# Optimization experiments

Hardware: AMD Instinct MI355X
Metric: run time of the kernel (lower is better)

Reference implementation:

```python
import jax, jax.numpy as jnp
import numpy as np

D_MODEL = 1024
N_HEADS = 16


def setup_inputs() -> dict:
    key = jax.random.key(0)
    ks = jax.random.split(key, 5)
    B, T, C = 4, 2048, D_MODEL
    x = jax.random.normal(ks[0], (B, T, C), dtype=jnp.float32)
    W_attn = jax.random.normal(ks[1], (C, 3 * C), dtype=jnp.float32) * (1.0 / np.sqrt(C))
    b_attn = jnp.zeros((3 * C,), dtype=jnp.float32)
    W_proj = jax.random.normal(ks[2], (C, C), dtype=jnp.float32) * (1.0 / np.sqrt(C))
    b_proj = jnp.zeros((C,), dtype=jnp.float32)
    return {"x": x, "W_attn": W_attn, "b_attn": b_attn, "W_proj": W_proj, "b_proj": b_proj}


def reference(x, W_attn, b_attn, W_proj, b_proj):
    B, T, C = x.shape
    H = N_HEADS
    hd = C // H
    qkv = x @ W_attn + b_attn                      # [B,T,3C]
    q, k, v = jnp.split(qkv, 3, axis=2)
    # [B,T,C] -> [B,H,T,hd]
    q = q.reshape(B, T, H, hd).transpose(0, 2, 1, 3)
    k = k.reshape(B, T, H, hd).transpose(0, 2, 1, 3)
    v = v.reshape(B, T, H, hd).transpose(0, 2, 1, 3)
    scale = 1.0 / jnp.sqrt(jnp.float32(hd))
    attn = jnp.einsum('bhqd,bhkd->bhqk', q, k) * scale
    causal = jnp.tril(jnp.ones((T, T), dtype=bool))
    attn = jnp.where(causal[None, None], attn, -jnp.inf)
    w = jax.nn.softmax(attn, axis=-1)
    ctx = jnp.einsum('bhqk,bhkd->bhqd', w, v)      # [B,H,T,hd]
    ctx = ctx.transpose(0, 2, 1, 3).reshape(B, T, C)
    return ctx @ W_proj + b_proj
```

## Files before the change

kernel.cpp:

```cpp
#include <hip/hip_runtime.h>
#include <hip/hip_bf16.h>

typedef __bf16 bf16x8 __attribute__((ext_vector_type(8)));
typedef __bf16 bf16x4 __attribute__((ext_vector_type(4)));
typedef float f32x4 __attribute__((ext_vector_type(4)));

#define MFMA(A, B, C) __builtin_amdgcn_mfma_f32_16x16x32_bf16((A), (B), (C), 0, 0, 0)

#if __has_builtin(__builtin_amdgcn_exp2f)
#define EXP2(x) __builtin_amdgcn_exp2f(x)
#else
#define EXP2(x) exp2f(x)
#endif

#define T_SEQ 2048
#define BATCH 4
#define CDIM  1024
#define HEADS 16
#define HD    64
#define MROWS (BATCH * T_SEQ)
#define QK_SCALE 0.18033688011112042f
#define KTILES (CDIM / 64)

__device__ __forceinline__ void async_ld16(const __bf16* g, __bf16* l) {
    __builtin_amdgcn_global_load_lds(
        (const __attribute__((address_space(1))) void*)g,
        (__attribute__((address_space(3))) void*)l, 16, 0, 0);
}

__global__ __launch_bounds__(256) void prep(const float* __restrict__ x,
                                            __bf16* __restrict__ xbf,
                                            const float* __restrict__ Wa,
                                            __bf16* __restrict__ Wat)
{
    __shared__ float tile[32][33];
    const int bid = blockIdx.x;
    if (bid < 4096) {
        long i = ((long)bid * 256 + threadIdx.x) * 8;
        f32x4 f0 = ((const f32x4*)(x + i))[0];
        f32x4 f1 = ((const f32x4*)(x + i))[1];
        bf16x8 v;
#pragma unroll
        for (int j = 0; j < 4; j++) { v[j] = (__bf16)f0[j]; v[4 + j] = (__bf16)f1[j]; }
        *(bf16x8*)(xbf + i) = v;
    } else {
        const int bb = bid - 4096;
        const int tx = threadIdx.x & 31, ty = threadIdx.x >> 5;
        const int c0 = (bb % 96) * 32, r0 = (bb / 96) * 32;
#pragma unroll
        for (int i = 0; i < 4; i++)
            tile[ty + i * 8][tx] = Wa[(long)(r0 + ty + i * 8) * (3 * CDIM) + c0 + tx];
        __syncthreads();
#pragma unroll
        for (int i = 0; i < 4; i++)
            Wat[(long)(c0 + ty + i * 8) * CDIM + r0 + tx] = (__bf16)tile[tx][ty + i * 8];
    }
}

__global__ __launch_bounds__(256) void conv_transpose(const float* __restrict__ src,
                                                      __bf16* __restrict__ dst,
                                                      int R, int C)
{
    __shared__ float tile[32][33];
    int c0 = blockIdx.x * 32, r0 = blockIdx.y * 32;
    int tx = threadIdx.x, ty = threadIdx.y;
#pragma unroll
    for (int i = 0; i < 4; i++)
        tile[ty + i * 8][tx] = src[(long)(r0 + ty + i * 8) * C + c0 + tx];
    __syncthreads();
#pragma unroll
    for (int i = 0; i < 4; i++)
        dst[(long)(c0 + ty + i * 8) * R + r0 + tx] = (__bf16)tile[tx][ty + i * 8];
}


#define QS_ALO(p, kt)                                                            \
    do {                                                                         \
        async_ld16(Asrc + (long)(kt) * 64, &Ab[p][sdst]);                        \
        async_ld16(Asrc + (long)128 * CDIM + (kt) * 64, &Ab[p][8192 + sdst]);    \
    } while (0)
#define QS_AHI(p, kt)                                                            \
    do {                                                                         \
        async_ld16(Asrc + (long)64 * CDIM + (kt) * 64, &Ab[p][4096 + sdst]);     \
        async_ld16(Asrc + (long)192 * CDIM + (kt) * 64, &Ab[p][12288 + sdst]);   \
    } while (0)
#define QS_B(p, kt)                                                              \
    do {                                                                         \
        async_ld16(Bsrc + (long)(kt) * 64, &Bb[p][sdst]);                        \
        async_ld16(Bsrc + (long)64 * CDIM + (kt) * 64, &Bb[p][4096 + sdst]);     \
        async_ld16(Bsrc + (long)128 * CDIM + (kt) * 64, &Bb[p][8192 + sdst]);    \
    } while (0)

__global__ __launch_bounds__(512, 2) void gemm_qkv(const __bf16* __restrict__ A,
                                                   const __bf16* __restrict__ Bt,
                                                   const float* __restrict__ bias,
                                                   __bf16* __restrict__ C,
                                                   __bf16* __restrict__ vt)
{
    __shared__ __attribute__((aligned(16))) __bf16 Ab[2][256 * 64];
    __shared__ __attribute__((aligned(16))) __bf16 Bb[2][192 * 64];

    const int bid = (int)blockIdx.x;
    const int swz = (bid & 7) * 64 + (bid >> 3);
    const int n0 = (swz & 15) * 192;
    const int m0 = (swz >> 4) * 256;

    const int t = threadIdx.x;
    const int wave = t >> 6, lane = t & 63;
    const int quad = lane >> 4, l15 = lane & 15;
    const int wm = wave >> 2, wn = wave & 3;

    const int srow = t >> 3;
    const int scol = ((t & 7) * 8) ^ ((srow & 7) << 3);
    const int sdst = srow * 64 + (t & 7) * 8;
    const __bf16* Asrc = A + (long)(m0 + srow) * CDIM + scol;
    const __bf16* Bsrc = Bt + (long)(n0 + srow) * CDIM + scol;

    const int kx0 = (quad * 8) ^ ((l15 & 7) << 3);
    const int kx1 = (32 + quad * 8) ^ ((l15 & 7) << 3);
    const int aro = (wm * 128 + l15) * 64;
    const int bro = (wn * 48 + l15) * 64;

    f32x4 acc[8][3] = {};
    bf16x8 A0[4][2], A1[4][2], B0[2][2], B1[2];

    QS_ALO(0, 0); QS_AHI(0, 0); QS_B(0, 0);
    QS_ALO(1, 1); QS_AHI(1, 1); QS_B(1, 1);
    asm volatile("s_waitcnt vmcnt(7)" ::: "memory");
    __builtin_amdgcn_s_barrier();
#pragma unroll
    for (int mf = 0; mf < 4; mf++) {
        A0[mf][0] = *(const bf16x8*)&Ab[0][aro + mf * 1024 + kx0];
        A0[mf][1] = *(const bf16x8*)&Ab[0][aro + mf * 1024 + kx1];
    }
#pragma unroll
    for (int nf = 0; nf < 2; nf++) {
        B0[nf][0] = *(const bf16x8*)&Bb[0][bro + nf * 1024 + kx0];
        B0[nf][1] = *(const bf16x8*)&Bb[0][bro + nf * 1024 + kx1];
    }

#pragma unroll 2
    for (int kt = 0; kt < KTILES; ++kt) {
        const int cur = kt & 1, nxt = cur ^ 1;

#pragma unroll
        for (int mf = 0; mf < 4; mf++) {
            A1[mf][0] = *(const bf16x8*)&Ab[cur][aro + 4096 + mf * 1024 + kx0];
            A1[mf][1] = *(const bf16x8*)&Ab[cur][aro + 4096 + mf * 1024 + kx1];
        }
        __builtin_amdgcn_s_barrier();
        asm volatile("s_waitcnt lgkmcnt(8)");
        __builtin_amdgcn_sched_barrier(0);
        __builtin_amdgcn_s_setprio(1);
#pragma unroll
        for (int mf = 0; mf < 4; mf++)
#pragma unroll
            for (int nf = 0; nf < 2; nf++) {
                acc[mf][nf] = MFMA(A0[mf][0], B0[nf][0], acc[mf][nf]);
                acc[mf][nf] = MFMA(A0[mf][1], B0[nf][1], acc[mf][nf]);
            }
        __builtin_amdgcn_s_setprio(0);
        __builtin_amdgcn_s_barrier();

        B1[0] = *(const bf16x8*)&Bb[cur][bro + 2048 + kx0];
        B1[1] = *(const bf16x8*)&Bb[cur][bro + 2048 + kx1];
        if (kt + 2 < KTILES) QS_ALO(cur, kt + 2);
        __builtin_amdgcn_s_barrier();
        asm volatile("s_waitcnt lgkmcnt(2)");
        __builtin_amdgcn_sched_barrier(0);
        __builtin_amdgcn_s_setprio(1);
#pragma unroll
        for (int mf = 0; mf < 4; mf++)
#pragma unroll
            for (int nf = 0; nf < 2; nf++) {
                acc[4 + mf][nf] = MFMA(A1[mf][0], B0[nf][0], acc[4 + mf][nf]);
                acc[4 + mf][nf] = MFMA(A1[mf][1], B0[nf][1], acc[4 + mf][nf]);
            }
        __builtin_amdgcn_s_setprio(0);
        if (kt + 2 < KTILES) { asm volatile("s_waitcnt vmcnt(2)" ::: "memory"); }
        else                 { asm volatile("s_waitcnt vmcnt(0)" ::: "memory"); }
        __builtin_amdgcn_s_barrier();

        if (kt + 2 < KTILES) QS_AHI(cur, kt + 2);
        if (kt + 1 < KTILES) {
#pragma unroll
            for (int nf = 0; nf < 2; nf++) {
                B0[nf][0] = *(const bf16x8*)&Bb[nxt][bro + nf * 1024 + kx0];
                B0[nf][1] = *(const bf16x8*)&Bb[nxt][bro + nf * 1024 + kx1];
            }
        }
        __builtin_amdgcn_s_barrier();
        asm volatile("s_waitcnt lgkmcnt(4)");
        __builtin_amdgcn_sched_barrier(0);
        __builtin_amdgcn_s_setprio(1);
#pragma unroll
        for (int mf = 0; mf < 4; mf++) {
            acc[mf][2] = MFMA(A0[mf][0], B1[0], acc[mf][2]);
            acc[mf][2] = MFMA(A0[mf][1], B1[1], acc[mf][2]);
        }
        __builtin_amdgcn_s_setprio(0);
        __builtin_amdgcn_s_barrier();

        if (kt + 2 < KTILES) QS_B(cur, kt + 2);
        if (kt + 1 < KTILES) {
#pragma unroll
            for (int mf = 0; mf < 4; mf++) {
                A0[mf][0] = *(const bf16x8*)&Ab[nxt][aro + mf * 1024 + kx0];
                A0[mf][1] = *(const bf16x8*)&Ab[nxt][aro + mf * 1024 + kx1];
            }
        }
        __builtin_amdgcn_s_barrier();
        asm volatile("s_waitcnt lgkmcnt(8)");
        __builtin_amdgcn_sched_barrier(0);
        __builtin_amdgcn_s_setprio(1);
#pragma unroll
        for (int mf = 0; mf < 4; mf++) {
            acc[4 + mf][2] = MFMA(A1[mf][0], B1[0], acc[4 + mf][2]);
            acc[4 + mf][2] = MFMA(A1[mf][1], B1[1], acc[4 + mf][2]);
        }
        __builtin_amdgcn_s_setprio(0);
        __builtin_amdgcn_s_barrier();
    }

    const int bB = m0 >> 11;
    const int tb = (m0 & (T_SEQ - 1)) + wm * 128;
#pragma unroll
    for (int mf = 0; mf < 8; mf++) {
#pragma unroll
        for (int nf = 0; nf < 3; nf++) {
            const int colb = n0 + wn * 48 + nf * 16;
            const int col = colb + l15;
            const float bv = bias[col];
            if (colb >= 2 * CDIM) {
                __bf16* vdst = vt + (long)(bB * CDIM + col - 2 * CDIM) * T_SEQ
                             + tb + (mf >> 2) * 64 + (mf & 3) * 16 + quad * 4;
                bf16x4 pv;
#pragma unroll
                for (int r = 0; r < 4; r++) pv[r] = (__bf16)(acc[mf][nf][r] + bv);
                *(bf16x4*)vdst = pv;
            } else {
                const float sc = (col < CDIM) ? QK_SCALE : 1.0f;
#pragma unroll
                for (int r = 0; r < 4; r++) {
                    const int row = m0 + wm * 128 + (mf >> 2) * 64 + (mf & 3) * 16 + quad * 4 + r;
                    C[(long)row * (3 * CDIM) + col] = (__bf16)((acc[mf][nf][r] + bv) * sc);
                }
            }
        }
    }
}

#define PS_A(p, kt)                                                              \
    do {                                                                         \
        async_ld16(Asrc + (long)(kt) * 64, &Ab[p][sdst]);                        \
        async_ld16(Asrc + (long)64 * (3 * CDIM) + (kt) * 64, &Ab[p][4096 + sdst]); \
    } while (0)
#define PS_B(p, kt)                                                              \
    do {                                                                         \
        async_ld16(Bsrc + (long)(kt) * 64, &Bb[p][sdst]);                        \
        async_ld16(Bsrc + (long)64 * CDIM + (kt) * 64, &Bb[p][4096 + sdst]);     \
        async_ld16(Bsrc + (long)128 * CDIM + (kt) * 64, &Bb[p][8192 + sdst]);    \
        async_ld16(Bsrc + (long)192 * CDIM + (kt) * 64, &Bb[p][12288 + sdst]);   \
    } while (0)

__global__ __launch_bounds__(512, 2) void gemm_proj(const __bf16* __restrict__ A,
                                                    const __bf16* __restrict__ Bt,
                                                    const float* __restrict__ bias,
                                                    float* __restrict__ C)
{
    __shared__ __attribute__((aligned(16))) __bf16 Ab[2][128 * 64];
    __shared__ __attribute__((aligned(16))) __bf16 Bb[2][256 * 64];

    const int bid = (int)blockIdx.x;
    const int swz = (bid & 7) * 32 + (bid >> 3);
    const int n0 = (swz & 3) * 256;
    const int m0 = (swz >> 2) * 128;

    const int t = threadIdx.x;
    const int wave = t >> 6, lane = t & 63;
    const int quad = lane >> 4, l15 = lane & 15;
    const int wm = wave >> 2, wn = wave & 3;

    const int srow = t >> 3;
    const int scol = ((t & 7) * 8) ^ ((srow & 7) << 3);
    const int sdst = srow * 64 + (t & 7) * 8;
    const __bf16* Asrc = A + (long)(m0 + srow) * (3 * CDIM) + scol;
    const __bf16* Bsrc = Bt + (long)(n0 + srow) * CDIM + scol;

    const int kx0 = (quad * 8) ^ ((l15 & 7) << 3);
    const int kx1 = (32 + quad * 8) ^ ((l15 & 7) << 3);
    const int aro = (wm * 64 + l15) * 64;
    const int bro = (wn * 64 + l15) * 64;

    f32x4 acc[4][4] = {};
    bf16x8 A0[2][2], A1[2][2], B0[2][2], B1[2][2];

    PS_A(0, 0); PS_B(0, 0);
    PS_A(1, 1); PS_B(1, 1);
    asm volatile("s_waitcnt vmcnt(6)" ::: "memory");
    __builtin_amdgcn_s_barrier();
#pragma unroll
    for (int mf = 0; mf < 2; mf++) {
        A0[mf][0] = *(const bf16x8*)&Ab[0][aro + mf * 1024 + kx0];
        A0[mf][1] = *(const bf16x8*)&Ab[0][aro + mf * 1024 + kx1];
    }
#pragma unroll
    for (int nf = 0; nf < 2; nf++) {
        B0[nf][0] = *(const bf16x8*)&Bb[0][bro + nf * 1024 + kx0];
        B0[nf][1] = *(const bf16x8*)&Bb[0][bro + nf * 1024 + kx1];
    }

#pragma unroll 2
    for (int kt = 0; kt < KTILES; ++kt) {
        const int cur = kt & 1, nxt = cur ^ 1;

#pragma unroll
        for (int mf = 0; mf < 2; mf++) {
            A1[mf][0] = *(const bf16x8*)&Ab[cur][aro + 2048 + mf * 1024 + kx0];
            A1[mf][1] = *(const bf16x8*)&Ab[cur][aro + 2048 + mf * 1024 + kx1];
        }
        __builtin_amdgcn_s_barrier();
        asm volatile("s_waitcnt lgkmcnt(4)");
        __builtin_amdgcn_sched_barrier(0);
        __builtin_amdgcn_s_setprio(1);
#pragma unroll
        for (int mf = 0; mf < 2; mf++)
#pragma unroll
            for (int nf = 0; nf < 2; nf++) {
                acc[mf][nf] = MFMA(A0[mf][0], B0[nf][0], acc[mf][nf]);
                acc[mf][nf] = MFMA(A0[mf][1], B0[nf][1], acc[mf][nf]);
            }
        __builtin_amdgcn_s_setprio(0);
        __builtin_amdgcn_s_barrier();

#pragma unroll
        for (int nf = 0; nf < 2; nf++) {
            B1[nf][0] = *(const bf16x8*)&Bb[cur][bro + 2048 + nf * 1024 + kx0];
            B1[nf][1] = *(const bf16x8*)&Bb[cur][bro + 2048 + nf * 1024 + kx1];
        }
        __builtin_amdgcn_s_barrier();
        asm volatile("s_waitcnt lgkmcnt(4)");
        __builtin_amdgcn_sched_barrier(0);
        __builtin_amdgcn_s_setprio(1);
#pragma unroll
        for (int mf = 0; mf < 2; mf++)
#pragma unroll
            for (int nf = 0; nf < 2; nf++) {
                acc[2 + mf][nf] = MFMA(A1[mf][0], B0[nf][0], acc[2 + mf][nf]);
                acc[2 + mf][nf] = MFMA(A1[mf][1], B0[nf][1], acc[2 + mf][nf]);
            }
        __builtin_amdgcn_s_setprio(0);
        asm volatile("s_waitcnt vmcnt(0)" ::: "memory");
        __builtin_amdgcn_s_barrier();

        if (kt + 2 < KTILES) PS_A(cur, kt + 2);
        if (kt + 1 < KTILES) {
#pragma unroll
            for (int nf = 0; nf < 2; nf++) {
                B0[nf][0] = *(const bf16x8*)&Bb[nxt][bro + nf * 1024 + kx0];
                B0[nf][1] = *(const bf16x8*)&Bb[nxt][bro + nf * 1024 + kx1];
            }
        }
        __builtin_amdgcn_s_barrier();
        asm volatile("s_waitcnt lgkmcnt(4)");
        __builtin_amdgcn_sched_barrier(0);
        __builtin_amdgcn_s_setprio(1);
#pragma unroll
        for (int mf = 0; mf < 2; mf++)
#pragma unroll
            for (int nf = 0; nf < 2; nf++) {
                acc[mf][2 + nf] = MFMA(A0[mf][0], B1[nf][0], acc[mf][2 + nf]);
                acc[mf][2 + nf] = MFMA(A0[mf][1], B1[nf][1], acc[mf][2 + nf]);
            }
        __builtin_amdgcn_s_setprio(0);
        __builtin_amdgcn_s_barrier();

        if (kt + 2 < KTILES) PS_B(cur, kt + 2);
        if (kt + 1 < KTILES) {
#pragma unroll
            for (int mf = 0; mf < 2; mf++) {
                A0[mf][0] = *(const bf16x8*)&Ab[nxt][aro + mf * 1024 + kx0];
                A0[mf][1] = *(const bf16x8*)&Ab[nxt][aro + mf * 1024 + kx1];
            }
        }
        __builtin_amdgcn_s_barrier();
        asm volatile("s_waitcnt lgkmcnt(4)");
        __builtin_amdgcn_sched_barrier(0);
        __builtin_amdgcn_s_setprio(1);
#pragma unroll
        for (int mf = 0; mf < 2; mf++)
#pragma unroll
            for (int nf = 0; nf < 2; nf++) {
                acc[2 + mf][2 + nf] = MFMA(A1[mf][0], B1[nf][0], acc[2 + mf][2 + nf]);
                acc[2 + mf][2 + nf] = MFMA(A1[mf][1], B1[nf][1], acc[2 + mf][2 + nf]);
            }
        __builtin_amdgcn_s_setprio(0);
        __builtin_amdgcn_s_barrier();
    }

#pragma unroll
    for (int mf = 0; mf < 4; mf++) {
#pragma unroll
        for (int nf = 0; nf < 4; nf++) {
            const int col = n0 + wn * 64 + (nf >> 1) * 32 + (nf & 1) * 16 + l15;
            const float bv = bias[col];
#pragma unroll
            for (int r = 0; r < 4; r++) {
                const int row = m0 + wm * 64 + (mf >> 1) * 32 + (mf & 1) * 16 + quad * 4 + r;
                C[(long)row * CDIM + col] = acc[mf][nf][r] + bv;
            }
        }
    }
}

__global__ __launch_bounds__(256) void attn_kernel(__bf16* qkv,
                                                   const __bf16* __restrict__ vt)
{
    __shared__ __attribute__((aligned(16))) __bf16 Ks[2][64 * 32];
    __shared__ __attribute__((aligned(16))) __bf16 Vts[2][64 * 32];
    __shared__ __attribute__((aligned(16))) __bf16 Ps[8][16 * 72];

    const int bh = blockIdx.x;
    const int b = bh >> 4, h = bh & 15;
    const int qt = (int)gridDim.y - 1 - (int)blockIdx.y;
    const int q0 = qt * 128;
    const int t = threadIdx.x;
    const int wave = t >> 6, lane = t & 63;
    const int quad = lane >> 4, l15 = lane & 15;

    bf16x8 qfr[2][2];
#pragma unroll
    for (int f = 0; f < 2; f++) {
        const __bf16* qb = qkv + (long)(b * T_SEQ + q0 + f * 64 + wave * 16 + l15) * (3 * CDIM) + h * HD;
        qfr[f][0] = *(const bf16x8*)(qb + quad * 8);
        qfr[f][1] = *(const bf16x8*)(qb + 32 + quad * 8);
    }

    bf16x8 vone;
#pragma unroll
    for (int j = 0; j < 8; j++) vone[j] = (__bf16)1.0f;

    f32x4 Oacc[2][4] = {};
    f32x4 lacc[2] = {};

    const __bf16* kbase = qkv + (long)(b * T_SEQ + (t >> 2)) * (3 * CDIM)
                          + CDIM + h * HD + (t & 3) * 8;
    const __bf16* vbase = vt + ((long)bh * HD + (t >> 2)) * T_SEQ + (t & 3) * 8;

    const int ntiles = (q0 + 128) / 64;
    for (int kt = 0; kt < ntiles; kt++) {
        const __bf16* kp = kbase + (long)kt * 64 * (3 * CDIM);
        async_ld16(kp,      &Ks[0][t * 8]);
        async_ld16(kp + 32, &Ks[1][t * 8]);
        const __bf16* vp = vbase + kt * 64;
        async_ld16(vp,      &Vts[0][t * 8]);
        async_ld16(vp + 32, &Vts[1][t * 8]);
        __syncthreads();

#pragma unroll
        for (int c = 0; c < 4; c++) {
            bf16x8 kf0 = *(const bf16x8*)&Ks[0][(c * 16 + l15) * 32 + quad * 8];
            bf16x8 kf1 = *(const bf16x8*)&Ks[1][(c * 16 + l15) * 32 + quad * 8];
#pragma unroll
            for (int f = 0; f < 2; f++) {
                f32x4 z = {};
                z = MFMA(kf0, qfr[f][0], z);
                z = MFMA(kf1, qfr[f][1], z);
                const int qbf = q0 + f * 64 + wave * 16;
                const int qg = qbf + l15;
                const int kvb = kt * 64 + c * 16 + quad * 4;
                bf16x4 pk;
                if (kt * 64 + 63 > qbf) {
#pragma unroll
                    for (int r = 0; r < 4; r++) {
                        float v = (kvb + r > qg) ? -1e30f : z[r];
                        pk[r] = (__bf16)EXP2(v);
                    }
                } else {
#pragma unroll
                    for (int r = 0; r < 4; r++)
                        pk[r] = (__bf16)EXP2(z[r]);
                }
                *(bf16x4*)&Ps[wave * 2 + f][l15 * 72 + c * 16 + quad * 4] = pk;
            }
        }

        __threadfence_block();

        bf16x8 pf[2][2];
#pragma unroll
        for (int f = 0; f < 2; f++) {
            pf[f][0] = *(const bf16x8*)&Ps[wave * 2 + f][l15 * 72 + quad * 8];
            pf[f][1] = *(const bf16x8*)&Ps[wave * 2 + f][l15 * 72 + 32 + quad * 8];
            lacc[f] = MFMA(pf[f][0], vone, lacc[f]);
            lacc[f] = MFMA(pf[f][1], vone, lacc[f]);
        }
#pragma unroll
        for (int n = 0; n < 4; n++) {
            bf16x8 vf0 = *(const bf16x8*)&Vts[0][(n * 16 + l15) * 32 + quad * 8];
            bf16x8 vf1 = *(const bf16x8*)&Vts[1][(n * 16 + l15) * 32 + quad * 8];
#pragma unroll
            for (int f = 0; f < 2; f++) {
                Oacc[f][n] = MFMA(pf[f][0], vf0, Oacc[f][n]);
                Oacc[f][n] = MFMA(pf[f][1], vf1, Oacc[f][n]);
            }
        }
        __syncthreads();
    }

#pragma unroll
    for (int f = 0; f < 2; f++)
#pragma unroll
        for (int n = 0; n < 4; n++) {
            int col = h * HD + n * 16 + l15;
#pragma unroll
            for (int r = 0; r < 4; r++) {
                int row = q0 + f * 64 + wave * 16 + quad * 4 + r;
                float val = Oacc[f][n][r] / lacc[f][r];
                qkv[(long)(b * T_SEQ + row) * (3 * CDIM) + col] = (__bf16)val;
            }
        }
}

extern "C" void kernel_launch(void* const* d_in, const int* in_sizes, int n_in,
                              void* d_out, int out_size, void* d_ws, size_t ws_size,
                              hipStream_t stream) {
    (void)in_sizes; (void)n_in; (void)out_size; (void)ws_size;
    const float* x  = (const float*)d_in[0];
    const float* Wa = (const float*)d_in[1];
    const float* ba = (const float*)d_in[2];
    const float* Wp = (const float*)d_in[3];
    const float* bp = (const float*)d_in[4];
    float* out = (float*)d_out;

    char* ws = (char*)d_ws;
    __bf16* qkv = (__bf16*)(ws);
    __bf16* vt  = (__bf16*)(ws + 50331648);
    __bf16* Wpt = (__bf16*)(ws + 50331648);
    __bf16* xbf = (__bf16*)d_out;
    __bf16* Wat = (__bf16*)((char*)d_out + 16777216);

    prep<<<dim3(4096 + 3072), 256, 0, stream>>>(x, xbf, Wa, Wat);

    gemm_qkv<<<dim3(512), 512, 0, stream>>>(xbf, Wat, ba, qkv, vt);

    attn_kernel<<<dim3(BATCH * HEADS, T_SEQ / 128), 256, 0, stream>>>(qkv, vt);

    conv_transpose<<<dim3(CDIM / 32, CDIM / 32), dim3(32, 8), 0, stream>>>(Wp, Wpt, CDIM, CDIM);

    gemm_proj<<<dim3(256), 512, 0, stream>>>(qkv, Wpt, bp, out);
}
```

Measured before the change: 249.8 us.

## Fold Wproj transpose into prep and stage V-transpose stores through LDS

New measurement: 251.4 us. Within noise of the previous version (+0.7%).

```diff
diff --git a/kernel.cpp b/kernel.cpp
--- a/kernel.cpp
+++ b/kernel.cpp
@@ -31,7 +31,9 @@
 __global__ __launch_bounds__(256) void prep(const float* __restrict__ x,
                                             __bf16* __restrict__ xbf,
                                             const float* __restrict__ Wa,
-                                            __bf16* __restrict__ Wat)
+                                            __bf16* __restrict__ Wat,
+                                            const float* __restrict__ Wp,
+                                            __bf16* __restrict__ qkv)
 {
     __shared__ float tile[32][33];
     const int bid = blockIdx.x;
@@ -43,7 +45,7 @@
 #pragma unroll
         for (int j = 0; j < 4; j++) { v[j] = (__bf16)f0[j]; v[4 + j] = (__bf16)f1[j]; }
         *(bf16x8*)(xbf + i) = v;
-    } else {
+    } else if (bid < 7168) {
         const int bb = bid - 4096;
         const int tx = threadIdx.x & 31, ty = threadIdx.x >> 5;
         const int c0 = (bb % 96) * 32, r0 = (bb / 96) * 32;
@@ -54,23 +56,19 @@
 #pragma unroll
         for (int i = 0; i < 4; i++)
             Wat[(long)(c0 + ty + i * 8) * CDIM + r0 + tx] = (__bf16)tile[tx][ty + i * 8];
-    }
-}
-
-__global__ __launch_bounds__(256) void conv_transpose(const float* __restrict__ src,
-                                                      __bf16* __restrict__ dst,
-                                                      int R, int C)
-{
-    __shared__ float tile[32][33];
-    int c0 = blockIdx.x * 32, r0 = blockIdx.y * 32;
-    int tx = threadIdx.x, ty = threadIdx.y;
-#pragma unroll
-    for (int i = 0; i < 4; i++)
-        tile[ty + i * 8][tx] = src[(long)(r0 + ty + i * 8) * C + c0 + tx];
-    __syncthreads();
-#pragma unroll
-    for (int i = 0; i < 4; i++)
-        dst[(long)(c0 + ty + i * 8) * R + r0 + tx] = (__bf16)tile[tx][ty + i * 8];
+    } else {
+        const int bb = bid - 7168;
+        const int tx = threadIdx.x & 31, ty = threadIdx.x >> 5;
+        const int c0 = (bb % 32) * 32, r0 = (bb / 32) * 32;
+#pragma unroll
+        for (int i = 0; i < 4; i++)
+            tile[ty + i * 8][tx] = Wp[(long)(r0 + ty + i * 8) * CDIM + c0 + tx];
+        __syncthreads();
+#pragma unroll
+        for (int i = 0; i < 4; i++)
+            qkv[(long)(c0 + ty + i * 8) * (3 * CDIM) + 2 * CDIM + r0 + tx] =
+                (__bf16)tile[tx][ty + i * 8];
+    }
 }
 
 
@@ -222,30 +220,57 @@
         __builtin_amdgcn_s_barrier();
     }
 
-    const int bB = m0 >> 11;
-    const int tb = (m0 & (T_SEQ - 1)) + wm * 128;
 #pragma unroll
     for (int mf = 0; mf < 8; mf++) {
 #pragma unroll
         for (int nf = 0; nf < 3; nf++) {
             const int colb = n0 + wn * 48 + nf * 16;
+            if (colb >= 2 * CDIM) continue;
             const int col = colb + l15;
             const float bv = bias[col];
-            if (colb >= 2 * CDIM) {
-                __bf16* vdst = vt + (long)(bB * CDIM + col - 2 * CDIM) * T_SEQ
-                             + tb + (mf >> 2) * 64 + (mf & 3) * 16 + quad * 4;
-                bf16x4 pv;
-#pragma unroll
-                for (int r = 0; r < 4; r++) pv[r] = (__bf16)(acc[mf][nf][r] + bv);
-                *(bf16x4*)vdst = pv;
-            } else {
-                const float sc = (col < CDIM) ? QK_SCALE : 1.0f;
-#pragma unroll
-                for (int r = 0; r < 4; r++) {
-                    const int row = m0 + wm * 128 + (mf >> 2) * 64 + (mf & 3) * 16 + quad * 4 + r;
-                    C[(long)row * (3 * CDIM) + col] = (__bf16)((acc[mf][nf][r] + bv) * sc);
+            const float sc = (col < CDIM) ? QK_SCALE : 1.0f;
+#pragma unroll
+            for (int r = 0; r < 4; r++) {
+                const int row = m0 + wm * 128 + (mf >> 2) * 64 + (mf & 3) * 16 + quad * 4 + r;
+                C[(long)row * (3 * CDIM) + col] = (__bf16)((acc[mf][nf][r] + bv) * sc);
+            }
+        }
+    }
+
+    if (n0 >= 1920) {
+        asm volatile("s_waitcnt lgkmcnt(0)" ::: "memory");
+        __builtin_amdgcn_s_barrier();
+        __bf16* vsc = &Ab[0][0] + wave * 3456;
+        const int bB = m0 >> 11;
+        const int tb = (m0 & (T_SEQ - 1)) + wm * 128;
+#pragma unroll
+        for (int mh = 0; mh < 2; mh++) {
+#pragma unroll
+            for (int mf4 = 0; mf4 < 4; mf4++) {
+#pragma unroll
+                for (int nf = 0; nf < 3; nf++) {
+                    const int colb = n0 + wn * 48 + nf * 16;
+                    if (colb < 2 * CDIM) continue;
+                    const float bv = bias[colb + l15];
+                    bf16x4 pv;
+#pragma unroll
+                    for (int r = 0; r < 4; r++)
+                        pv[r] = (__bf16)(acc[mh * 4 + mf4][nf][r] + bv);
+                    *(bf16x4*)&vsc[(nf * 16 + l15) * 72 + mf4 * 16 + quad * 4] = pv;
                 }
             }
+            __threadfence_block();
+#pragma unroll
+            for (int p = 0; p < 6; p++) {
+                const int c = p * 8 + (lane >> 3);
+                const int colg = n0 + wn * 48 + c;
+                if (colg >= 2 * CDIM) {
+                    bf16x8 vv = *(const bf16x8*)&vsc[c * 72 + (lane & 7) * 8];
+                    *(bf16x8*)(vt + (long)(bB * CDIM + colg - 2 * CDIM) * T_SEQ
+                               + tb + mh * 64 + (lane & 7) * 8) = vv;
+                }
+            }
+            __threadfence_block();
         }
     }
 }
@@ -258,13 +283,12 @@
 #define PS_B(p, kt)                                                              \
     do {                                                                         \
         async_ld16(Bsrc + (long)(kt) * 64, &Bb[p][sdst]);                        \
-        async_ld16(Bsrc + (long)64 * CDIM + (kt) * 64, &Bb[p][4096 + sdst]);     \
-        async_ld16(Bsrc + (long)128 * CDIM + (kt) * 64, &Bb[p][8192 + sdst]);    \
-        async_ld16(Bsrc + (long)192 * CDIM + (kt) * 64, &Bb[p][12288 + sdst]);   \
+        async_ld16(Bsrc + (long)64 * (3 * CDIM) + (kt) * 64, &Bb[p][4096 + sdst]); \
+        async_ld16(Bsrc + (long)128 * (3 * CDIM) + (kt) * 64, &Bb[p][8192 + sdst]); \
+        async_ld16(Bsrc + (long)192 * (3 * CDIM) + (kt) * 64, &Bb[p][12288 + sdst]); \
     } while (0)
 
 __global__ __launch_bounds__(512, 2) void gemm_proj(const __bf16* __restrict__ A,
-                                                    const __bf16* __restrict__ Bt,
                                                     const float* __restrict__ bias,
                                                     float* __restrict__ C)
 {
@@ -285,7 +309,7 @@
     const int scol = ((t & 7) * 8) ^ ((srow & 7) << 3);
     const int sdst = srow * 64 + (t & 7) * 8;
     const __bf16* Asrc = A + (long)(m0 + srow) * (3 * CDIM) + scol;
-    const __bf16* Bsrc = Bt + (long)(n0 + srow) * CDIM + scol;
+    const __bf16* Bsrc = A + (long)(n0 + srow) * (3 * CDIM) + 2 * CDIM + scol;
 
     const int kx0 = (quad * 8) ^ ((l15 & 7) << 3);
     const int kx1 = (32 + quad * 8) ^ ((l15 & 7) << 3);
@@ -536,17 +560,14 @@
     char* ws = (char*)d_ws;
     __bf16* qkv = (__bf16*)(ws);
     __bf16* vt  = (__bf16*)(ws + 50331648);
-    __bf16* Wpt = (__bf16*)(ws + 50331648);
     __bf16* xbf = (__bf16*)d_out;
     __bf16* Wat = (__bf16*)((char*)d_out + 16777216);
 
-    prep<<<dim3(4096 + 3072), 256, 0, stream>>>(x, xbf, Wa, Wat);
+    prep<<<dim3(8192), 256, 0, stream>>>(x, xbf, Wa, Wat, Wp, qkv);
 
     gemm_qkv<<<dim3(512), 512, 0, stream>>>(xbf, Wat, ba, qkv, vt);
 
     attn_kernel<<<dim3(BATCH * HEADS, T_SEQ / 128), 256, 0, stream>>>(qkv, vt);
 
-    conv_transpose<<<dim3(CDIM / 32, CDIM / 32), dim3(32, 8), 0, stream>>>(Wp, Wpt, CDIM, CDIM);
-
-    gemm_proj<<<dim3(256), 512, 0, stream>>>(qkv, Wpt, bp, out);
+    gemm_proj<<<dim3(256), 512, 0, stream>>>(qkv, bp, out);
 }
```
